# Performance work log

Hardware: AMD Instinct MI355X
Metric: run time of the kernel (lower is better)

## Reference

```python
import jax, jax.numpy as jnp
import numpy as np

FULL_SCALE = 128
TOPK = 8
R = 0.5


def setup_inputs() -> dict:
    key = jax.random.key(0)
    ks = jax.random.split(key, 6)
    B, Na, Nb, D = 4, 8192, 8192, 256
    return {
        "a_feats": jax.random.normal(ks[0], (B, Na, D), jnp.float32),
        "b_feats": jax.random.normal(ks[1], (B, Nb, D), jnp.float32),
        "coords_a": jax.random.randint(ks[2], (B, Na, 3), 0, 2048, jnp.int32),
        "coords_b": jax.random.randint(ks[3], (B, Nb, 3), 0, 2048, jnp.int32),
        "w1": jax.random.normal(ks[4], (D, 2 * D), jnp.float32) / np.sqrt(2 * D),
        "b1": jnp.zeros((D,), jnp.float32),
        "w2": jax.random.normal(ks[5], (D, D), jnp.float32) / np.sqrt(D),
        "b2": jnp.zeros((D,), jnp.float32),
    }


def _cli_one(af, bf, ca, cb, w1, b1, w2, b2):
    # af:[Na,D] bf:[Nb,D] ca:[Na,3] cb:[Nb,3] (float coords, already //16)
    # torch.cdist (euclidean) / full_scale
    d2 = (jnp.sum(ca * ca, 1)[:, None] + jnp.sum(cb * cb, 1)[None, :]
          - 2.0 * ca @ cb.T)
    dist = jnp.sqrt(jnp.maximum(d2, 0.0)) / FULL_SCALE  # [Na, Nb]
    neg_d, idx = jax.lax.top_k(-dist, TOPK)             # smallest k distances
    dw = R - jnp.clip(-neg_d, 0.0, R)                   # [Na, k]
    nb = bf[idx]                                        # gather [Na, k, D]
    x = jnp.concatenate([nb, af[:, None, :] - nb], axis=-1)  # [Na, k, 2D]
    h = jax.nn.relu(jnp.einsum('nkf,df->nkd', x, w1) + b1) * dw[..., None]
    o = jnp.einsum('nkd,ed->nke', h, w2) + b2           # [Na, k, D]
    return jnp.sum(o, axis=1)                           # [Na, D]


def reference(a_feats, b_feats, coords_a, coords_b, w1, b1, w2, b2):
    ca = (coords_a // 16).astype(jnp.float32)
    cb = (coords_b // 16).astype(jnp.float32)
    fuse = jax.vmap(lambda af, bf, x, y: _cli_one(af, bf, x, y, w1, b1, w2, b2))(
        a_feats, b_feats, ca, cb)
    # ME.cat(a, tmp): concatenate features along channel dim
    return jnp.concatenate([a_feats, fuse], axis=-1)  # [B, Na, 2D]
```

## Files before the change

kernel.cpp:

```cpp
#include <hip/hip_runtime.h>
#include <math.h>

typedef short short8_t __attribute__((ext_vector_type(8)));
typedef __bf16 bf16x8_t __attribute__((ext_vector_type(8)));
typedef float f32x4_t __attribute__((ext_vector_type(4)));

__device__ __forceinline__ float bf2f(unsigned short u) {
  unsigned v = ((unsigned)u) << 16;
  return __builtin_bit_cast(float, v);
}
__device__ __forceinline__ unsigned short f2bf(float f) {
  unsigned x = __builtin_bit_cast(unsigned, f);
  x += 0x7fffu + ((x >> 16) & 1u);
  return (unsigned short)(x >> 16);
}

#define NA 8192
#define NB 8192
#define NBATCH 4
#define DIM 256
#define NPTS (NBATCH * NA)
#define NCELL 2048
#define SUBL 8

__device__ __forceinline__ void kins(unsigned k[8], unsigned x) {
  unsigned c = x < k[7] ? x : k[7];
#pragma unroll
  for (int i = 6; i >= 0; i--) {
    unsigned hi = k[i] > c ? k[i] : c;
    c = k[i] < c ? k[i] : c;
    k[i + 1] = hi;
  }
  k[0] = c;
}

__global__ __launch_bounds__(256) void prep_weights(
    const float* __restrict__ w1, const float* __restrict__ w2,
    unsigned short* __restrict__ Wdiff, unsigned short* __restrict__ Wb,
    unsigned short* __restrict__ W2b, unsigned* __restrict__ bcnt,
    unsigned* __restrict__ acnt, unsigned* __restrict__ failcnt) {
  int d = blockIdx.x, t = threadIdx.x;
  float wa = w1[d * 512 + t];
  float wb = w1[d * 512 + 256 + t];
  Wdiff[d * 256 + t] = f2bf(wa - wb);
  Wb[d * 256 + t] = f2bf(wb);
  W2b[d * 256 + t] = f2bf(w2[d * 256 + t]);
  if (d < 8) {
    int i = d * 256 + t;
    bcnt[i] = 0;
    acnt[i] = 0;
    if (i == 0) *failcnt = 0;
  }
}

__global__ __launch_bounds__(256) void pack_count_ab(
    const int* __restrict__ coords_b, const int* __restrict__ coords_a,
    unsigned* __restrict__ bpk, unsigned* __restrict__ apk,
    unsigned* __restrict__ bcnt, unsigned* __restrict__ acnt) {
  int gi = blockIdx.x * 256 + threadIdx.x;
  const int isA = gi >= NPTS;
  const int i = gi & (NPTS - 1);
  const int* __restrict__ coords = isA ? coords_a : coords_b;
  unsigned* __restrict__ pk = isA ? apk : bpk;
  unsigned* __restrict__ cnt = isA ? acnt : bcnt;
  int x = (coords[(size_t)i * 3 + 0] >> 4) & 127;
  int y = (coords[(size_t)i * 3 + 1] >> 4) & 127;
  int z = (coords[(size_t)i * 3 + 2] >> 4) & 127;
  pk[i] = (unsigned)(x | (y << 7) | (z << 14));
  int cid = ((i >> 13) << 9) | ((x >> 4) << 6) | ((y >> 4) << 3) | (z >> 4);
  atomicAdd(cnt + cid, 1u);
}

__global__ __launch_bounds__(256) void scan_cells(
    const unsigned* __restrict__ bcnt, const unsigned* __restrict__ acnt,
    unsigned* __restrict__ boff, unsigned* __restrict__ aoff,
    unsigned* __restrict__ bcur, unsigned* __restrict__ acur) {
  __shared__ unsigned p[256];
  const int t = threadIdx.x;
  for (int tab = 0; tab < 2; tab++) {
    const unsigned* cnt = tab ? acnt : bcnt;
    unsigned* off = tab ? aoff : boff;
    unsigned* cur = tab ? acur : bcur;
    unsigned loc[8], sum = 0;
#pragma unroll
    for (int k = 0; k < 8; k++) { loc[k] = sum; sum += cnt[t * 8 + k]; }
    p[t] = sum;
    __syncthreads();
    for (int d = 1; d < 256; d <<= 1) {
      unsigned v = (t >= d) ? p[t - d] : 0u;
      __syncthreads();
      p[t] += v;
      __syncthreads();
    }
    unsigned base = (t == 0) ? 0u : p[t - 1];
#pragma unroll
    for (int k = 0; k < 8; k++) {
      unsigned o = base + loc[k];
      off[t * 8 + k] = o;
      cur[t * 8 + k] = o;
    }
    if (t == 255) off[2048] = base + sum;
    __syncthreads();
  }
}

__global__ __launch_bounds__(256) void scatter_ab(
    const unsigned* __restrict__ bpk, const unsigned* __restrict__ apk,
    unsigned* __restrict__ bcur, unsigned* __restrict__ acur,
    uint2* __restrict__ bout, uint2* __restrict__ aout) {
  int gi = blockIdx.x * 256 + threadIdx.x;
  const int isA = gi >= NPTS;
  const int i = gi & (NPTS - 1);
  const unsigned* __restrict__ pk = isA ? apk : bpk;
  unsigned* __restrict__ cur = isA ? acur : bcur;
  uint2* __restrict__ out = isA ? aout : bout;
  unsigned v = pk[i];
  int cx = (v & 127) >> 4, cy = ((v >> 7) & 127) >> 4, cz = ((v >> 14) & 127) >> 4;
  int cid = ((i >> 13) << 9) | (cx << 6) | (cy << 3) | cz;
  unsigned pos = atomicAdd(cur + cid, 1u);
  out[pos] = make_uint2(v, (unsigned)(i & 8191));
}

#define LDT 72
template <int F32IN>
__global__ __launch_bounds__(512) void gemm_wide(
    const void* __restrict__ Ain, const short* __restrict__ W,
    float* __restrict__ Cf, unsigned short* __restrict__ Cb,
    const float* __restrict__ bias, float bias_scale,
    int c_stride, int c_coloff, float* __restrict__ copyout) {
  __shared__ __attribute__((aligned(16))) short As[128 * LDT];
  __shared__ __attribute__((aligned(16))) short Bs[256 * LDT];
  const int tid = threadIdx.x;
  const int row0 = blockIdx.x * 128;
  const int w = tid >> 6, lane = tid & 63;
  const int wm = (w & 1) * 64, wn = (w >> 1) * 64;
  f32x4_t acc[4][4] = {};
  for (int k0 = 0; k0 < 256; k0 += 64) {
    if (F32IN) {
      const float* Af = (const float*)Ain;
#pragma unroll
      for (int i = 0; i < 2; i++) {
        int c = tid + 512 * i;
        int r = c >> 3, kc = (c & 7) * 8;
        const float* src = Af + (size_t)(row0 + r) * 256 + k0 + kc;
        float4 v0 = *(const float4*)src;
        float4 v1 = *(const float4*)(src + 4);
        short8_t vb;
        vb[0] = (short)f2bf(v0.x); vb[1] = (short)f2bf(v0.y);
        vb[2] = (short)f2bf(v0.z); vb[3] = (short)f2bf(v0.w);
        vb[4] = (short)f2bf(v1.x); vb[5] = (short)f2bf(v1.y);
        vb[6] = (short)f2bf(v1.z); vb[7] = (short)f2bf(v1.w);
        *(short8_t*)(As + r * LDT + kc) = vb;
        if (copyout) {
          float4* dst = (float4*)(copyout + (size_t)(row0 + r) * 512 + k0 + kc);
          dst[0] = v0;
          dst[1] = v1;
        }
      }
    } else {
      const short* Ab = (const short*)Ain;
#pragma unroll
      for (int i = 0; i < 2; i++) {
        int c = tid + 512 * i;
        int r = c >> 3, kc = (c & 7) * 8;
        *(short8_t*)(As + r * LDT + kc) =
            *(const short8_t*)(Ab + (size_t)(row0 + r) * 256 + k0 + kc);
      }
    }
#pragma unroll
    for (int i = 0; i < 4; i++) {
      int c = tid + 512 * i;
      int r = c >> 3, kc = (c & 7) * 8;
      *(short8_t*)(Bs + r * LDT + kc) =
          *(const short8_t*)(W + (size_t)r * 256 + k0 + kc);
    }
    __syncthreads();
#pragma unroll
    for (int kk = 0; kk < 64; kk += 32) {
      const int kof = kk + (lane >> 4) * 8;
      bf16x8_t af[4], bfr[4];
#pragma unroll
      for (int i = 0; i < 4; i++) {
        af[i] = __builtin_bit_cast(bf16x8_t,
            *(const short8_t*)(As + (wm + i * 16 + (lane & 15)) * LDT + kof));
        bfr[i] = __builtin_bit_cast(bf16x8_t,
            *(const short8_t*)(Bs + (wn + i * 16 + (lane & 15)) * LDT + kof));
      }
#pragma unroll
      for (int i = 0; i < 4; i++)
#pragma unroll
        for (int j = 0; j < 4; j++)
          acc[i][j] = __builtin_amdgcn_mfma_f32_16x16x32_bf16(
              af[i], bfr[j], acc[i][j], 0, 0, 0);
    }
    __syncthreads();
  }
#pragma unroll
  for (int i = 0; i < 4; i++) {
    int row = row0 + wm + i * 16 + ((lane >> 4) * 4);
#pragma unroll
    for (int j = 0; j < 4; j++) {
      int col = wn + j * 16 + (lane & 15);
      float bv = bias ? bias[col] * bias_scale : 0.f;
#pragma unroll
      for (int r = 0; r < 4; r++) {
        float v = acc[i][j][r] + bv;
        size_t off = (size_t)(row + r) * c_stride + c_coloff + col;
        if (Cf) Cf[off] = v;
        else Cb[off] = f2bf(v);
      }
    }
  }
}

__global__ __launch_bounds__(256) void topk_bins(
    const unsigned* __restrict__ boff, const uint2* __restrict__ bcj,
    const uint2* __restrict__ acj, int* __restrict__ idxb,
    float* __restrict__ dwb, unsigned* __restrict__ failcnt,
    unsigned* __restrict__ faillist) {
  const int tid = blockIdx.x * 256 + threadIdx.x;
  const int t = tid / SUBL;
  const int sub = tid & (SUBL - 1);
  const uint2 av = acj[t];
  const int batch = t >> 13;
  const int ax = av.x & 127, ay = (av.x >> 7) & 127, az = (av.x >> 14) & 127;
  const int cx = ax >> 4, cy = ay >> 4, cz = az >> 4;
  const int xlo = max(cx - 1, 0), xhi = min(cx + 1, 7);
  const int ylo = max(cy - 1, 0), yhi = min(cy + 1, 7);
  const int zlo = max(cz - 1, 0), zhi1 = min(cz + 1, 7) + 1;
  unsigned k[8];
#pragma unroll
  for (int s = 0; s < 8; s++) k[s] = 0xFFFFFFF8u + s;
  for (int nx = xlo; nx <= xhi; nx++) {
    for (int ny = ylo; ny <= yhi; ny++) {
      const int cb = (batch << 9) | (nx << 6) | (ny << 3);
      const int gs = (int)boff[cb + zlo];
      const int ge = (int)boff[cb + zhi1];
      for (int i = gs + sub; i < ge; i += SUBL) {
        const uint2 b = bcj[i];
        const int dx = ax - (int)(b.x & 127);
        const int dy = ay - (int)((b.x >> 7) & 127);
        const int dz = az - (int)((b.x >> 14) & 127);
        const unsigned d2 = (unsigned)(__mul24(dx, dx) + __mul24(dy, dy) +
                                       __mul24(dz, dz));
        kins(k, (d2 << 13) | b.y);
      }
    }
  }
  const int lane = threadIdx.x & 63;
#pragma unroll
  for (int half = 1; half < SUBL; half <<= 1) {
    unsigned o[8];
#pragma unroll
    for (int s = 0; s < 8; s++)
      o[s] = (unsigned)__shfl((int)k[s], lane ^ half, 64);
#pragma unroll
    for (int s = 0; s < 8; s++) kins(k, o[s]);
  }
  if (sub == 0) {
    const int g = (batch << 13) | (int)av.y;
#pragma unroll
    for (int s = 0; s < 8; s++) {
      unsigned key = k[s];
      idxb[(size_t)g * 8 + s] = (int)(key & 8191u);
      float dist = sqrtf((float)(key >> 13)) * (1.0f / 128.0f);
      dwb[(size_t)g * 8 + s] = 0.5f - fminf(dist, 0.5f);
    }
    if (k[7] >= (289u << 13)) {
      unsigned fp = atomicAdd(failcnt, 1u);
      faillist[fp] = (unsigned)g;
    }
  }
}

__global__ __launch_bounds__(256) void topk_fallback(
    const unsigned* __restrict__ failcnt, const unsigned* __restrict__ faillist,
    const uint2* __restrict__ bcj, const unsigned* __restrict__ apk,
    int* __restrict__ idxb, float* __restrict__ dwb) {
  __shared__ unsigned sk[4 * 8];
  const int tid = threadIdx.x;
  const int wv = tid >> 6, lane = tid & 63;
  const unsigned nf = *failcnt;
  for (unsigned fi = blockIdx.x; fi < nf; fi += gridDim.x) {
    const unsigned g = faillist[fi];
    const int batch = (int)(g >> 13);
    const unsigned av = apk[g];
    const int ax = av & 127, ay = (av >> 7) & 127, az = (av >> 14) & 127;
    const uint2* pb = bcj + ((size_t)batch << 13);
    unsigned k[8];
#pragma unroll
    for (int s = 0; s < 8; s++) k[s] = 0xFFFFFFF8u + s;
#pragma unroll 8
    for (int i = tid; i < NB; i += 256) {
      const uint2 b = pb[i];
      const int dx = ax - (int)(b.x & 127);
      const int dy = ay - (int)((b.x >> 7) & 127);
      const int dz = az - (int)((b.x >> 14) & 127);
      const unsigned d2 = (unsigned)(__mul24(dx, dx) + __mul24(dy, dy) +
                                     __mul24(dz, dz));
      kins(k, (d2 << 13) | b.y);
    }
#pragma unroll
    for (int half = 32; half >= 1; half >>= 1) {
      unsigned o[8];
#pragma unroll
      for (int s = 0; s < 8; s++)
        o[s] = (unsigned)__shfl((int)k[s], lane ^ half, 64);
#pragma unroll
      for (int s = 0; s < 8; s++) kins(k, o[s]);
    }
    if (lane == 0) {
#pragma unroll
      for (int s = 0; s < 8; s++) sk[wv * 8 + s] = k[s];
    }
    __syncthreads();
    if (tid == 0) {
#pragma unroll
      for (int w = 1; w < 4; w++)
#pragma unroll
        for (int s = 0; s < 8; s++) kins(k, sk[w * 8 + s]);
#pragma unroll
      for (int s = 0; s < 8; s++) {
        unsigned key = k[s];
        idxb[(size_t)g * 8 + s] = (int)(key & 8191u);
        float dist = sqrtf((float)(key >> 13)) * (1.0f / 128.0f);
        dwb[(size_t)g * 8 + s] = 0.5f - fminf(dist, 0.5f);
      }
    }
    __syncthreads();
  }
}

__global__ __launch_bounds__(256) void fuse_kernel(
    const unsigned short* __restrict__ Pa, const unsigned short* __restrict__ Pb,
    const uint2* __restrict__ acj, const int* __restrict__ idxb,
    const float* __restrict__ dwb, unsigned short* __restrict__ H) {
  const int t = blockIdx.x * 4 + (threadIdx.x >> 6);
  const int lane = threadIdx.x & 63;
  const int batch = t >> 13;
  const uint2 av = acj[t];
  const int g = (batch << 13) | (int)av.y;
  const size_t fo = (size_t)g * 256 + lane * 4;
  ushort4 pav = *(const ushort4*)(Pa + fo);
  const float pa0 = bf2f(pav.x), pa1 = bf2f(pav.y), pa2 = bf2f(pav.z),
              pa3 = bf2f(pav.w);
  float h0 = 0.f, h1 = 0.f, h2 = 0.f, h3 = 0.f;
  const size_t bbase = (size_t)(batch << 13) * 256;
#pragma unroll
  for (int k = 0; k < 8; k++) {
    const int j = idxb[(size_t)g * 8 + k];
    const float w = dwb[(size_t)g * 8 + k];
    const ushort4 pbv =
        *(const ushort4*)(Pb + bbase + (size_t)j * 256 + lane * 4);
    h0 += fmaxf(pa0 + bf2f(pbv.x), 0.f) * w;
    h1 += fmaxf(pa1 + bf2f(pbv.y), 0.f) * w;
    h2 += fmaxf(pa2 + bf2f(pbv.z), 0.f) * w;
    h3 += fmaxf(pa3 + bf2f(pbv.w), 0.f) * w;
  }
  ushort4 hv;
  hv.x = f2bf(h0); hv.y = f2bf(h1); hv.z = f2bf(h2); hv.w = f2bf(h3);
  *(ushort4*)(H + fo) = hv;
}

extern "C" void kernel_launch(void* const* d_in, const int* in_sizes, int n_in,
                              void* d_out, int out_size, void* d_ws,
                              size_t ws_size, hipStream_t stream) {
  const float* a_feats = (const float*)d_in[0];
  const float* b_feats = (const float*)d_in[1];
  const int* coords_a = (const int*)d_in[2];
  const int* coords_b = (const int*)d_in[3];
  const float* w1 = (const float*)d_in[4];
  const float* b1 = (const float*)d_in[5];
  const float* w2 = (const float*)d_in[6];
  const float* b2 = (const float*)d_in[7];
  float* outp = (float*)d_out;

  char* p = (char*)d_ws;
  auto take = [&](size_t bytes) {
    char* r = p;
    p += (bytes + 255) & ~(size_t)255;
    return r;
  };
  unsigned short* Pa = (unsigned short*)take((size_t)NPTS * DIM * 2);
  unsigned short* Pb = (unsigned short*)take((size_t)NPTS * DIM * 2);
  unsigned short* Hb = (unsigned short*)take((size_t)NPTS * DIM * 2);
  int* idxb = (int*)take((size_t)NPTS * 8 * 4);
  float* dwb = (float*)take((size_t)NPTS * 8 * 4);
  unsigned* bpk = (unsigned*)take((size_t)NPTS * 4);
  unsigned* apk = (unsigned*)take((size_t)NPTS * 4);
  unsigned* bcnt = (unsigned*)take(NCELL * 4);
  unsigned* acnt = (unsigned*)take(NCELL * 4);
  unsigned* bcur = (unsigned*)take(NCELL * 4);
  unsigned* acur = (unsigned*)take(NCELL * 4);
  unsigned* boff = (unsigned*)take((NCELL + 1) * 4);
  unsigned* aoff = (unsigned*)take((NCELL + 1) * 4);
  uint2* bcj = (uint2*)take((size_t)NPTS * 8);
  uint2* acj = (uint2*)take((size_t)NPTS * 8);
  unsigned* failcnt = (unsigned*)take(256);
  unsigned* faillist = (unsigned*)take((size_t)NPTS * 4);
  unsigned short* Wdiff = (unsigned short*)take(256 * 256 * 2);
  unsigned short* Wb16 = (unsigned short*)take(256 * 256 * 2);
  unsigned short* W2b = (unsigned short*)take(256 * 256 * 2);

  prep_weights<<<256, 256, 0, stream>>>(w1, w2, Wdiff, Wb16, W2b, bcnt, acnt,
                                        failcnt);
  pack_count_ab<<<2 * NPTS / 256, 256, 0, stream>>>(coords_b, coords_a, bpk,
                                                    apk, bcnt, acnt);
  scan_cells<<<1, 256, 0, stream>>>(bcnt, acnt, boff, aoff, bcur, acur);
  scatter_ab<<<2 * NPTS / 256, 256, 0, stream>>>(bpk, apk, bcur, acur, bcj,
                                                 acj);

  gemm_wide<1><<<NPTS / 128, 512, 0, stream>>>(
      (const void*)a_feats, (const short*)Wb16, nullptr, Pa, b1, 1.0f, 256, 0,
      outp);
  gemm_wide<1><<<NPTS / 128, 512, 0, stream>>>(
      (const void*)b_feats, (const short*)Wdiff, nullptr, Pb, nullptr, 0.0f,
      256, 0, nullptr);

  topk_bins<<<NPTS * SUBL / 256, 256, 0, stream>>>(boff, bcj, acj, idxb, dwb,
                                                   failcnt, faillist);
  topk_fallback<<<256, 256, 0, stream>>>(failcnt, faillist, bcj, apk, idxb,
                                         dwb);

  fuse_kernel<<<NPTS / 4, 256, 0, stream>>>(Pa, Pb, acj, idxb, dwb, Hb);

  gemm_wide<0><<<NPTS / 128, 512, 0, stream>>>(
      (const void*)Hb, (const short*)W2b, outp, nullptr, b2, 8.0f, 512, 256,
      nullptr);
}
```

Before: 236.3 us.

## Shrink GEMM tiles to 64 rows and merge the two input GEMMs into one launch

The 128x256 tile GEMM with 512 threads becomes a 64x256 tile with 256 threads, where each wave owns a 64-column slice. The a_feats and b_feats projections are merged into a single launch that picks its operands by block index. The aim is to double the block count (512 blocks per GEMM, 1024 for the merged one) to fill the 256 CUs better and to cut one launch. In exchange, each block reloads the full 256x64 weight tile per k-step for only 64 rows, which doubles weight traffic per output row and lowers MFMA reuse of the B operand.

```diff
diff --git a/kernel.cpp b/kernel.cpp
--- a/kernel.cpp
+++ b/kernel.cpp
@@ -123,24 +123,22 @@
 
 #define LDT 72
 template <int F32IN>
-__global__ __launch_bounds__(512) void gemm_wide(
-    const void* __restrict__ Ain, const short* __restrict__ W,
+__device__ __forceinline__ void gemm64_body(
+    int rowblk, const void* __restrict__ Ain, const short* __restrict__ W,
     float* __restrict__ Cf, unsigned short* __restrict__ Cb,
-    const float* __restrict__ bias, float bias_scale,
-    int c_stride, int c_coloff, float* __restrict__ copyout) {
-  __shared__ __attribute__((aligned(16))) short As[128 * LDT];
-  __shared__ __attribute__((aligned(16))) short Bs[256 * LDT];
+    const float* __restrict__ bias, float bias_scale, int c_stride,
+    int c_coloff, float* __restrict__ copyout, short* As, short* Bs) {
   const int tid = threadIdx.x;
-  const int row0 = blockIdx.x * 128;
+  const int row0 = rowblk * 64;
   const int w = tid >> 6, lane = tid & 63;
-  const int wm = (w & 1) * 64, wn = (w >> 1) * 64;
+  const int wn = w * 64;
   f32x4_t acc[4][4] = {};
   for (int k0 = 0; k0 < 256; k0 += 64) {
     if (F32IN) {
       const float* Af = (const float*)Ain;
 #pragma unroll
       for (int i = 0; i < 2; i++) {
-        int c = tid + 512 * i;
+        int c = tid + 256 * i;
         int r = c >> 3, kc = (c & 7) * 8;
         const float* src = Af + (size_t)(row0 + r) * 256 + k0 + kc;
         float4 v0 = *(const float4*)src;
@@ -161,15 +159,15 @@
       const short* Ab = (const short*)Ain;
 #pragma unroll
       for (int i = 0; i < 2; i++) {
-        int c = tid + 512 * i;
+        int c = tid + 256 * i;
         int r = c >> 3, kc = (c & 7) * 8;
         *(short8_t*)(As + r * LDT + kc) =
             *(const short8_t*)(Ab + (size_t)(row0 + r) * 256 + k0 + kc);
       }
     }
 #pragma unroll
-    for (int i = 0; i < 4; i++) {
-      int c = tid + 512 * i;
+    for (int i = 0; i < 8; i++) {
+      int c = tid + 256 * i;
       int r = c >> 3, kc = (c & 7) * 8;
       *(short8_t*)(Bs + r * LDT + kc) =
           *(const short8_t*)(W + (size_t)r * 256 + k0 + kc);
@@ -182,7 +180,7 @@
 #pragma unroll
       for (int i = 0; i < 4; i++) {
         af[i] = __builtin_bit_cast(bf16x8_t,
-            *(const short8_t*)(As + (wm + i * 16 + (lane & 15)) * LDT + kof));
+            *(const short8_t*)(As + (i * 16 + (lane & 15)) * LDT + kof));
         bfr[i] = __builtin_bit_cast(bf16x8_t,
             *(const short8_t*)(Bs + (wn + i * 16 + (lane & 15)) * LDT + kof));
       }
@@ -197,7 +195,7 @@
   }
 #pragma unroll
   for (int i = 0; i < 4; i++) {
-    int row = row0 + wm + i * 16 + ((lane >> 4) * 4);
+    int row = row0 + i * 16 + ((lane >> 4) * 4);
 #pragma unroll
     for (int j = 0; j < 4; j++) {
       int col = wn + j * 16 + (lane & 15);
@@ -211,6 +209,34 @@
       }
     }
   }
+}
+
+__global__ __launch_bounds__(256, 3) void gemm_ab(
+    const float* __restrict__ a_feats, const float* __restrict__ b_feats,
+    const short* __restrict__ Wb16, const short* __restrict__ Wdiff,
+    unsigned short* __restrict__ Pa, unsigned short* __restrict__ Pb,
+    const float* __restrict__ b1, float* __restrict__ outp) {
+  __shared__ __attribute__((aligned(16))) short As[64 * LDT];
+  __shared__ __attribute__((aligned(16))) short Bs[256 * LDT];
+  const int nb = NPTS / 64;
+  const int isB = blockIdx.x >= nb;
+  const int rowblk = isB ? (blockIdx.x - nb) : blockIdx.x;
+  const float* Af = isB ? b_feats : a_feats;
+  const short* W = isB ? Wdiff : Wb16;
+  unsigned short* P = isB ? Pb : Pa;
+  const float* bias = isB ? nullptr : b1;
+  float* copy = isB ? nullptr : outp;
+  gemm64_body<1>(rowblk, (const void*)Af, W, nullptr, P, bias, 1.0f, 256, 0,
+                 copy, As, Bs);
+}
+
+__global__ __launch_bounds__(256, 3) void gemm_h(
+    const short* __restrict__ Hb, const short* __restrict__ W2b,
+    float* __restrict__ outp, const float* __restrict__ b2) {
+  __shared__ __attribute__((aligned(16))) short As[64 * LDT];
+  __shared__ __attribute__((aligned(16))) short Bs[256 * LDT];
+  gemm64_body<0>(blockIdx.x, (const void*)Hb, W2b, outp, nullptr, b2, 8.0f,
+                 512, 256, nullptr, As, Bs);
 }
 
 __global__ __launch_bounds__(256) void topk_bins(
@@ -410,12 +436,10 @@
   scatter_ab<<<2 * NPTS / 256, 256, 0, stream>>>(bpk, apk, bcur, acur, bcj,
                                                  acj);
 
-  gemm_wide<1><<<NPTS / 128, 512, 0, stream>>>(
-      (const void*)a_feats, (const short*)Wb16, nullptr, Pa, b1, 1.0f, 256, 0,
-      outp);
-  gemm_wide<1><<<NPTS / 128, 512, 0, stream>>>(
-      (const void*)b_feats, (const short*)Wdiff, nullptr, Pb, nullptr, 0.0f,
-      256, 0, nullptr);
+  gemm_ab<<<2 * NPTS / 64, 256, 0, stream>>>(a_feats, b_feats,
+                                             (const short*)Wb16,
+                                             (const short*)Wdiff, Pa, Pb, b1,
+                                             outp);
 
   topk_bins<<<NPTS * SUBL / 256, 256, 0, stream>>>(boff, bcj, acj, idxb, dwb,
                                                    failcnt, faillist);
@@ -424,7 +448,6 @@
 
   fuse_kernel<<<NPTS / 4, 256, 0, stream>>>(Pa, Pb, acj, idxb, dwb, Hb);
 
-  gemm_wide<0><<<NPTS / 128, 512, 0, stream>>>(
-      (const void*)Hb, (const short*)W2b, outp, nullptr, b2, 8.0f, 512, 256,
-      nullptr);
-}
+  gemm_h<<<NPTS / 64, 256, 0, stream>>>((const short*)Hb, (const short*)W2b,
+                                        outp, b2);
+}
```

Measured after the change: 227.0 us. -4.0%, faster.
